# Optimization experiments

Measured on AMD Instinct MI355X. Metric: run time of the kernel, lower is better.

The kernel has to match this reference:

```python
import jax, jax.numpy as jnp
import numpy as np

EPS = 1e-8
H = 4      # n_heads
W = 64     # mem_word_length


def _split_controls(controls):
    # per-head partition: [W, W, W, 1, 1, 3, 1]
    B = controls.shape[0]
    sizes = [W, W, W, 1, 1, 3, 1]
    parts, pos = [], 0
    for s in sizes:
        n = H * s
        parts.append(controls[:, pos:pos + n].reshape(B, H, s))
        pos += n
    return parts  # keys, erase_vec, write_vec, betas, gates, shifts, gammas


def _address_memory(memory, keys, betas, gates, shifts, gammas, prev_weights):
    keys = jnp.tanh(keys)                      # [B,H,W]
    betas = jax.nn.softplus(betas)             # [B,H,1]
    gates = jax.nn.sigmoid(gates)              # [B,H,1]
    shifts = jax.nn.softmax(shifts, axis=-1)   # [B,H,3]
    gammas = 1.0 + jax.nn.softplus(gammas)     # [B,H,1]

    # cosine similarity: [B,H,N]
    dots = jnp.einsum('bhw,bnw->bhn', keys, memory)
    norm = jnp.linalg.norm(keys, axis=-1, keepdims=True) \
         * jnp.linalg.norm(memory, axis=-1)[:, None, :]
    scores = dots / (norm + EPS)

    w_content = jax.nn.softmax(scores * betas, axis=-1)            # [B,H,N]
    w_interp = gates * w_content + (1.0 - gates) * prev_weights    # [B,H,N]

    # circular 3-tap shift: out[n] = s0*w[n-1] + s1*w[n] + s2*w[n+1]
    w_shift = (shifts[..., 0:1] * jnp.roll(w_interp, 1, axis=-1)
             + shifts[..., 1:2] * w_interp
             + shifts[..., 2:3] * jnp.roll(w_interp, -1, axis=-1))

    w_sharp = w_shift ** gammas
    return w_sharp / (jnp.sum(w_sharp, axis=-1, keepdims=True) + EPS)


def reference(memory, controls, prev_weights):
    keys, erase_vec, write_vec, betas, gates, shifts, gammas = _split_controls(controls)
    write_dist = _address_memory(memory, keys, betas, gates, shifts, gammas, prev_weights)  # [B,H,N]
    write_data = jnp.tanh(write_vec)       # [B,H,W]
    erase_data = jax.nn.sigmoid(erase_vec) # [B,H,W]

    # erase: prod over heads of (1 - w[b,h,n]*e[b,h,w]) -> [B,N,W]
    erase_matrix = jnp.prod(1.0 - write_dist[:, :, :, None] * erase_data[:, :, None, :], axis=1)
    update_matrix = jnp.einsum('bhn,bhw->bnw', write_dist, write_data)
    return memory * erase_matrix + update_matrix


def setup_inputs() -> dict:
    key = jax.random.key(0)
    k1, k2, k3 = jax.random.split(key, 3)
    B, N = 64, 8192
    memory = jax.random.normal(k1, (B, N, W), dtype=jnp.float32)
    controls = jax.random.normal(k2, (B, H * (3 * W + 6)), dtype=jnp.float32)
    prev_weights = jax.random.uniform(k3, (B, H, N), dtype=jnp.float32)
    return {"memory": memory, "controls": controls, "prev_weights": prev_weights}
```

## Files before the change

### kernel.cpp

```cpp
#include <hip/hip_runtime.h>
#include <math.h>

#define EPS 1e-8f

typedef float nfloat4 __attribute__((ext_vector_type(4)));

__device__ __forceinline__ float softplus_f(float x) {
    return (x > 20.0f) ? x : log1pf(expf(x));
}
__device__ __forceinline__ float sigmoid_f(float x) {
    return 1.0f / (1.0f + expf(-x));
}


__global__ __launch_bounds__(256)
void score_kernel(const float* __restrict__ memory,
                  const float* __restrict__ controls,
                  float* __restrict__ scores, int N)
{
    int b = blockIdx.y;
    int nbase = blockIdx.x * 128;
    int t = threadIdx.x;
    int rq = t >> 4;
    int lane = t & 15;

    __shared__ float kk[256];
    __shared__ float betas_s[4], knorm_s[4];
    __shared__ float sc[4][128];

    const float* c = controls + (size_t)b * 792;

    {
        int h = t >> 6, w = t & 63;
        float kt = tanhf(c[h * 64 + w]);
        kk[h * 64 + w] = kt;
        float nsq = kt * kt;
        #pragma unroll
        for (int m = 1; m < 64; m <<= 1) nsq += __shfl_xor(nsq, m, 64);
        if (w == 0) knorm_s[h] = sqrtf(nsq);
        if (t < 4)  betas_s[t] = softplus_f(c[768 + t]);
    }
    __syncthreads();

    float4 k4[4];
    #pragma unroll
    for (int h = 0; h < 4; h++) k4[h] = ((const float4*)(kk + h * 64))[lane];
    float beta_l[4], knorm_l[4];
    #pragma unroll
    for (int h = 0; h < 4; h++) { beta_l[h] = betas_s[h]; knorm_l[h] = knorm_s[h]; }

    float4 m4[8];
    #pragma unroll
    for (int j = 0; j < 8; j++) {
        int n = nbase + rq + 16 * j;
        m4[j] = ((const float4*)(memory + ((size_t)b * N + n) * 64))[lane];
    }

    #pragma unroll
    for (int j = 0; j < 8; j++) {
        float nsq = m4[j].x * m4[j].x + m4[j].y * m4[j].y
                  + m4[j].z * m4[j].z + m4[j].w * m4[j].w;
        float d[4];
        #pragma unroll
        for (int h = 0; h < 4; h++) {
            d[h] = m4[j].x * k4[h].x + m4[j].y * k4[h].y
                 + m4[j].z * k4[h].z + m4[j].w * k4[h].w;
        }
        #pragma unroll
        for (int m = 1; m < 16; m <<= 1) {
            nsq += __shfl_xor(nsq, m, 64);
            #pragma unroll
            for (int h = 0; h < 4; h++) d[h] += __shfl_xor(d[h], m, 64);
        }
        if (lane == 0) {
            float mn = sqrtf(nsq);
            int row = rq + 16 * j;
            #pragma unroll
            for (int h = 0; h < 4; h++)
                sc[h][row] = beta_l[h] * d[h] / (mn * knorm_l[h] + EPS);
        }
    }
    __syncthreads();
    #pragma unroll
    for (int k = 0; k < 2; k++) {
        int idx = t + k * 256;
        int h = idx >> 7, i = idx & 127;
        scores[((size_t)b * 4 + h) * N + nbase + i] = sc[h][i];
    }
}

__device__ __forceinline__ float block_reduce_sum(float v, float* red) {
    #pragma unroll
    for (int m = 1; m < 64; m <<= 1) v += __shfl_xor(v, m, 64);
    int wid = threadIdx.x >> 6;
    __syncthreads();
    if ((threadIdx.x & 63) == 0) red[wid] = v;
    __syncthreads();
    float r = red[0];
    #pragma unroll
    for (int i = 1; i < 16; i++) r += red[i];
    return r;
}
__device__ __forceinline__ float block_reduce_max(float v, float* red) {
    #pragma unroll
    for (int m = 1; m < 64; m <<= 1) v = fmaxf(v, __shfl_xor(v, m, 64));
    int wid = threadIdx.x >> 6;
    __syncthreads();
    if ((threadIdx.x & 63) == 0) red[wid] = v;
    __syncthreads();
    float r = red[0];
    #pragma unroll
    for (int i = 1; i < 16; i++) r = fmaxf(r, red[i]);
    return r;
}

__global__ __launch_bounds__(1024)
void weights_kernel(float* __restrict__ scores,
                    const float* __restrict__ prev,
                    const float* __restrict__ controls, int N)
{
    int bh = blockIdx.x;
    int b = bh >> 2, h = bh & 3;
    int t = threadIdx.x;
    const float* c = controls + (size_t)b * 792;

    float gate  = sigmoid_f(c[772 + h]);
    float r0 = c[776 + h * 3 + 0];
    float r1 = c[776 + h * 3 + 1];
    float r2 = c[776 + h * 3 + 2];
    float rmx = fmaxf(r0, fmaxf(r1, r2));
    float e0 = expf(r0 - rmx), e1 = expf(r1 - rmx), e2 = expf(r2 - rmx);
    float sinv = 1.0f / (e0 + e1 + e2);
    float s0 = e0 * sinv, s1 = e1 * sinv, s2 = e2 * sinv;
    float gamma = 1.0f + softplus_f(c[788 + h]);

    __shared__ float wi_s[8192];
    __shared__ float red[16];

    float* srow = scores + (size_t)bh * N;
    const float* prow = prev + (size_t)bh * N;
    int half = N >> 1;
    int i0 = 4 * t, i1 = half + 4 * t;

    float4 sa = ((const float4*)srow)[t];
    float4 sb = ((const float4*)srow)[half / 4 + t];
    float4 pa = ((const float4*)prow)[t];
    float4 pb = ((const float4*)prow)[half / 4 + t];

    float mx = fmaxf(fmaxf(fmaxf(sa.x, sa.y), fmaxf(sa.z, sa.w)),
                     fmaxf(fmaxf(sb.x, sb.y), fmaxf(sb.z, sb.w)));
    mx = block_reduce_max(mx, red);

    float ea[4] = { __expf(sa.x - mx), __expf(sa.y - mx), __expf(sa.z - mx), __expf(sa.w - mx) };
    float eb[4] = { __expf(sb.x - mx), __expf(sb.y - mx), __expf(sb.z - mx), __expf(sb.w - mx) };
    float lsum = ea[0] + ea[1] + ea[2] + ea[3] + eb[0] + eb[1] + eb[2] + eb[3];
    float S = block_reduce_sum(lsum, red);
    float invS = 1.0f / S;

    float og = 1.0f - gate;
    float pv_a[4] = { pa.x, pa.y, pa.z, pa.w };
    float pv_b[4] = { pb.x, pb.y, pb.z, pb.w };
    #pragma unroll
    for (int k = 0; k < 4; k++) {
        wi_s[i0 + k] = gate * (ea[k] * invS) + og * pv_a[k];
        wi_s[i1 + k] = gate * (eb[k] * invS) + og * pv_b[k];
    }
    __syncthreads();

    float wsv[8]; float lsum2 = 0.0f;
    #pragma unroll
    for (int cc = 0; cc < 2; cc++) {
        int base = (cc == 0) ? i0 : i1;
        #pragma unroll
        for (int k = 0; k < 4; k++) {
            int i = base + k;
            int im1 = (i == 0) ? (N - 1) : (i - 1);
            int ip1 = (i == N - 1) ? 0 : (i + 1);
            float ws = s0 * wi_s[im1] + s1 * wi_s[i] + s2 * wi_s[ip1];
            float wp = __expf(gamma * __logf(ws));
            wsv[cc * 4 + k] = wp; lsum2 += wp;
        }
    }
    float T = block_reduce_sum(lsum2, red);
    float invT = 1.0f / (T + EPS);

    float4 oa = make_float4(wsv[0] * invT, wsv[1] * invT, wsv[2] * invT, wsv[3] * invT);
    float4 ob = make_float4(wsv[4] * invT, wsv[5] * invT, wsv[6] * invT, wsv[7] * invT);
    ((float4*)srow)[t] = oa;
    ((float4*)srow)[half / 4 + t] = ob;
}

__global__ __launch_bounds__(256)
void output_kernel(const float* __restrict__ memory,
                   const float* __restrict__ wdist,
                   const float* __restrict__ controls,
                   float* __restrict__ out, int N)
{
    int t = threadIdx.x;
    int blocksPerB = N >> 7;
    int b = blockIdx.x / blocksPerB;
    int nbase = (blockIdx.x % blocksPerB) << 7;

    __shared__ float es[256], wv[256], wd_s[512];
    const float* c = controls + (size_t)b * 792;
    es[t] = sigmoid_f(c[256 + t]);
    wv[t] = tanhf(c[512 + t]);
    #pragma unroll
    for (int k = 0; k < 2; k++) {
        int idx = t + k * 256;
        int h = idx >> 7, i = idx & 127;
        wd_s[idx] = wdist[((size_t)b * 4 + h) * N + nbase + i];
    }
    __syncthreads();

    int rq = t >> 4, lane = t & 15;

    float4 e4[4], w4[4];
    #pragma unroll
    for (int h = 0; h < 4; h++) {
        e4[h] = ((const float4*)(es + h * 64))[lane];
        w4[h] = ((const float4*)(wv + h * 64))[lane];
    }

    float4 m4[8];
    #pragma unroll
    for (int j = 0; j < 8; j++) {
        int n = nbase + rq + 16 * j;
        m4[j] = ((const float4*)(memory + ((size_t)b * N + n) * 64))[lane];
    }

    #pragma unroll
    for (int j = 0; j < 8; j++) {
        int row = rq + 16 * j;
        int n = nbase + row;
        float4 pe = make_float4(1.f, 1.f, 1.f, 1.f);
        float4 up = make_float4(0.f, 0.f, 0.f, 0.f);
        #pragma unroll
        for (int h = 0; h < 4; h++) {
            float f = wd_s[h * 128 + row];
            pe.x *= 1.0f - f * e4[h].x;  pe.y *= 1.0f - f * e4[h].y;
            pe.z *= 1.0f - f * e4[h].z;  pe.w *= 1.0f - f * e4[h].w;
            up.x += f * w4[h].x;  up.y += f * w4[h].y;
            up.z += f * w4[h].z;  up.w += f * w4[h].w;
        }
        nfloat4 o;
        o.x = m4[j].x * pe.x + up.x;
        o.y = m4[j].y * pe.y + up.y;
        o.z = m4[j].z * pe.z + up.z;
        o.w = m4[j].w * pe.w + up.w;
        nfloat4* op = ((nfloat4*)(out + ((size_t)b * N + n) * 64)) + lane;
        __builtin_nontemporal_store(o, op);
    }
}

extern "C" void kernel_launch(void* const* d_in, const int* in_sizes, int n_in,
                              void* d_out, int out_size, void* d_ws, size_t ws_size,
                              hipStream_t stream) {
    const float* memory   = (const float*)d_in[0];
    const float* controls = (const float*)d_in[1];
    const float* prev     = (const float*)d_in[2];
    float* out = (float*)d_out;

    int B = in_sizes[1] / 792;
    int N = in_sizes[0] / (B * 64);

    float* scores = (float*)d_ws;

    score_kernel<<<dim3(N / 128, B), 256, 0, stream>>>(memory, controls, scores, N);
    weights_kernel<<<B * 4, 1024, 0, stream>>>(scores, prev, controls, N);
    output_kernel<<<B * (N / 128), 256, 0, stream>>>(memory, scores, controls, out, N);
}
```

Baseline: 268.5 us.

## Drop softmax max pass and split weight stage across chunked blocks

Uses the fact that cosine similarity scaled by beta is bounded by beta, so exponentials are computed as exp(s-beta) directly in the score kernel, along with per-tile partial sums. This removes the global max reduction. The weights stage is split into many 2048-element chunks with halo loads and partial sharpening sums, and the final normalization moves into the output kernel. This increases parallelism for the sequential per-head stage, at the cost of extra partial-sum buffers and a small risk of underflow when beta is large.

Measured after the change: 263.8 us. No clear change (-1.7%).

```diff
diff --git a/kernel.cpp b/kernel.cpp
--- a/kernel.cpp
+++ b/kernel.cpp
@@ -16,13 +16,16 @@
 __global__ __launch_bounds__(256)
 void score_kernel(const float* __restrict__ memory,
                   const float* __restrict__ controls,
-                  float* __restrict__ scores, int N)
+                  float* __restrict__ evals,
+                  float* __restrict__ S_part, int N)
 {
     int b = blockIdx.y;
-    int nbase = blockIdx.x * 128;
+    int tile = blockIdx.x;
+    int nbase = tile * 128;
     int t = threadIdx.x;
     int rq = t >> 4;
     int lane = t & 15;
+    int ntiles = N >> 7;
 
     __shared__ float kk[256];
     __shared__ float betas_s[4], knorm_s[4];
@@ -76,53 +79,57 @@
             float mn = sqrtf(nsq);
             int row = rq + 16 * j;
             #pragma unroll
-            for (int h = 0; h < 4; h++)
-                sc[h][row] = beta_l[h] * d[h] / (mn * knorm_l[h] + EPS);
-        }
-    }
-    __syncthreads();
+            for (int h = 0; h < 4; h++) {
+                float s = beta_l[h] * d[h] / (mn * knorm_l[h] + EPS);
+                sc[h][row] = __expf(s - beta_l[h]);
+            }
+        }
+    }
+    __syncthreads();
+
     #pragma unroll
     for (int k = 0; k < 2; k++) {
         int idx = t + k * 256;
         int h = idx >> 7, i = idx & 127;
-        scores[((size_t)b * 4 + h) * N + nbase + i] = sc[h][i];
-    }
-}
-
-__device__ __forceinline__ float block_reduce_sum(float v, float* red) {
-    #pragma unroll
-    for (int m = 1; m < 64; m <<= 1) v += __shfl_xor(v, m, 64);
-    int wid = threadIdx.x >> 6;
-    __syncthreads();
-    if ((threadIdx.x & 63) == 0) red[wid] = v;
-    __syncthreads();
-    float r = red[0];
-    #pragma unroll
-    for (int i = 1; i < 16; i++) r += red[i];
-    return r;
-}
-__device__ __forceinline__ float block_reduce_max(float v, float* red) {
-    #pragma unroll
-    for (int m = 1; m < 64; m <<= 1) v = fmaxf(v, __shfl_xor(v, m, 64));
-    int wid = threadIdx.x >> 6;
-    __syncthreads();
-    if ((threadIdx.x & 63) == 0) red[wid] = v;
-    __syncthreads();
-    float r = red[0];
-    #pragma unroll
-    for (int i = 1; i < 16; i++) r = fmaxf(r, red[i]);
-    return r;
-}
-
-__global__ __launch_bounds__(1024)
-void weights_kernel(float* __restrict__ scores,
-                    const float* __restrict__ prev,
-                    const float* __restrict__ controls, int N)
+        evals[((size_t)b * 4 + h) * N + nbase + i] = sc[h][i];
+    }
+
+    {
+        int h = t >> 6, w = t & 63;
+        float v = sc[h][w] + sc[h][w + 64];
+        #pragma unroll
+        for (int m = 1; m < 64; m <<= 1) v += __shfl_xor(v, m, 64);
+        if (w == 0) S_part[((size_t)b * 4 + h) * ntiles + tile] = v;
+    }
+}
+
+__global__ __launch_bounds__(256)
+void shift_kernel(const float* __restrict__ evals,
+                  const float* __restrict__ prev,
+                  const float* __restrict__ controls,
+                  const float* __restrict__ S_part,
+                  float* __restrict__ wp,
+                  float* __restrict__ T_part, int N)
 {
-    int bh = blockIdx.x;
+    int CH = N >> 11;
+    int bh = blockIdx.x / CH;
+    int chunk = blockIdx.x - bh * CH;
     int b = bh >> 2, h = bh & 3;
     int t = threadIdx.x;
+    int ntiles = N >> 7;
     const float* c = controls + (size_t)b * 792;
+
+    __shared__ float wl[2050];
+    __shared__ float redm[4];
+    __shared__ float Ssh;
+
+    if (t < 64) {
+        float v = 0.0f;
+        for (int i = t; i < ntiles; i += 64) v += S_part[(size_t)bh * ntiles + i];
+        #pragma unroll
+        for (int m = 1; m < 64; m <<= 1) v += __shfl_xor(v, m, 64);
+        if (t == 0) Ssh = v;
+    }
 
     float gate  = sigmoid_f(c[772 + h]);
     float r0 = c[776 + h * 3 + 0];
@@ -134,65 +141,73 @@
     float s0 = e0 * sinv, s1 = e1 * sinv, s2 = e2 * sinv;
     float gamma = 1.0f + softplus_f(c[788 + h]);
 
-    __shared__ float wi_s[8192];
-    __shared__ float red[16];
-
-    float* srow = scores + (size_t)bh * N;
-    const float* prow = prev + (size_t)bh * N;
-    int half = N >> 1;
-    int i0 = 4 * t, i1 = half + 4 * t;
-
-    float4 sa = ((const float4*)srow)[t];
-    float4 sb = ((const float4*)srow)[half / 4 + t];
-    float4 pa = ((const float4*)prow)[t];
-    float4 pb = ((const float4*)prow)[half / 4 + t];
-
-    float mx = fmaxf(fmaxf(fmaxf(sa.x, sa.y), fmaxf(sa.z, sa.w)),
-                     fmaxf(fmaxf(sb.x, sb.y), fmaxf(sb.z, sb.w)));
-    mx = block_reduce_max(mx, red);
-
-    float ea[4] = { __expf(sa.x - mx), __expf(sa.y - mx), __expf(sa.z - mx), __expf(sa.w - mx) };
-    float eb[4] = { __expf(sb.x - mx), __expf(sb.y - mx), __expf(sb.z - mx), __expf(sb.w - mx) };
-    float lsum = ea[0] + ea[1] + ea[2] + ea[3] + eb[0] + eb[1] + eb[2] + eb[3];
-    float S = block_reduce_sum(lsum, red);
-    float invS = 1.0f / S;
-
+    const float* erow = evals + (size_t)bh * N;
+    const float* prow = prev  + (size_t)bh * N;
+    int base = chunk << 11;
+    int li = t << 3;
+
+    float4 ea = ((const float4*)(erow + base))[2 * t];
+    float4 eb = ((const float4*)(erow + base))[2 * t + 1];
+    float4 pa = ((const float4*)(prow + base))[2 * t];
+    float4 pb = ((const float4*)(prow + base))[2 * t + 1];
+
+    __syncthreads();
+    float invS = 1.0f / Ssh;
     float og = 1.0f - gate;
-    float pv_a[4] = { pa.x, pa.y, pa.z, pa.w };
-    float pv_b[4] = { pb.x, pb.y, pb.z, pb.w };
-    #pragma unroll
-    for (int k = 0; k < 4; k++) {
-        wi_s[i0 + k] = gate * (ea[k] * invS) + og * pv_a[k];
-        wi_s[i1 + k] = gate * (eb[k] * invS) + og * pv_b[k];
-    }
-    __syncthreads();
-
-    float wsv[8]; float lsum2 = 0.0f;
-    #pragma unroll
-    for (int cc = 0; cc < 2; cc++) {
-        int base = (cc == 0) ? i0 : i1;
-        #pragma unroll
-        for (int k = 0; k < 4; k++) {
-            int i = base + k;
-            int im1 = (i == 0) ? (N - 1) : (i - 1);
-            int ip1 = (i == N - 1) ? 0 : (i + 1);
-            float ws = s0 * wi_s[im1] + s1 * wi_s[i] + s2 * wi_s[ip1];
-            float wp = __expf(gamma * __logf(ws));
-            wsv[cc * 4 + k] = wp; lsum2 += wp;
-        }
-    }
-    float T = block_reduce_sum(lsum2, red);
-    float invT = 1.0f / (T + EPS);
-
-    float4 oa = make_float4(wsv[0] * invT, wsv[1] * invT, wsv[2] * invT, wsv[3] * invT);
-    float4 ob = make_float4(wsv[4] * invT, wsv[5] * invT, wsv[6] * invT, wsv[7] * invT);
-    ((float4*)srow)[t] = oa;
-    ((float4*)srow)[half / 4 + t] = ob;
+
+    float w[8];
+    w[0] = gate * ea.x * invS + og * pa.x;
+    w[1] = gate * ea.y * invS + og * pa.y;
+    w[2] = gate * ea.z * invS + og * pa.z;
+    w[3] = gate * ea.w * invS + og * pa.w;
+    w[4] = gate * eb.x * invS + og * pb.x;
+    w[5] = gate * eb.y * invS + og * pb.y;
+    w[6] = gate * eb.z * invS + og * pb.z;
+    w[7] = gate * eb.w * invS + og * pb.w;
+
+    #pragma unroll
+    for (int k = 0; k < 8; k++) wl[1 + li + k] = w[k];
+    if (t == 0) {
+        int g = base - 1; if (g < 0) g += N;
+        wl[0] = gate * erow[g] * invS + og * prow[g];
+    }
+    if (t == 255) {
+        int g = base + 2048; if (g >= N) g -= N;
+        wl[2049] = gate * erow[g] * invS + og * prow[g];
+    }
+    __syncthreads();
+
+    float nb[10];
+    nb[0] = wl[li];
+    #pragma unroll
+    for (int k = 0; k < 8; k++) nb[k + 1] = w[k];
+    nb[9] = wl[li + 9];
+
+    float o[8];
+    float acc = 0.0f;
+    #pragma unroll
+    for (int k = 0; k < 8; k++) {
+        float ws = s0 * nb[k] + s1 * nb[k + 1] + s2 * nb[k + 2];
+        float v = __expf(gamma * __logf(ws));
+        o[k] = v; acc += v;
+    }
+
+    #pragma unroll
+    for (int m = 1; m < 64; m <<= 1) acc += __shfl_xor(acc, m, 64);
+    if ((t & 63) == 0) redm[t >> 6] = acc;
+    __syncthreads();
+    if (t == 0) T_part[(size_t)bh * CH + chunk] = redm[0] + redm[1] + redm[2] + redm[3];
+
+    float4 oa = make_float4(o[0], o[1], o[2], o[3]);
+    float4 ob = make_float4(o[4], o[5], o[6], o[7]);
+    ((float4*)(wp + (size_t)bh * N + base))[2 * t] = oa;
+    ((float4*)(wp + (size_t)bh * N + base))[2 * t + 1] = ob;
 }
 
 __global__ __launch_bounds__(256)
 void output_kernel(const float* __restrict__ memory,
                    const float* __restrict__ wdist,
+                   const float* __restrict__ T_part,
                    const float* __restrict__ controls,
                    float* __restrict__ out, int N)
 {
@@ -200,16 +215,23 @@
     int blocksPerB = N >> 7;
     int b = blockIdx.x / blocksPerB;
     int nbase = (blockIdx.x % blocksPerB) << 7;
-
-    __shared__ float es[256], wv[256], wd_s[512];
+    int CH = N >> 11;
+
+    __shared__ float es[256], wv[256], wd_s[512], invT_s[4];
     const float* c = controls + (size_t)b * 792;
+    if (t < 4) {
+        float s = 0.0f;
+        for (int cc = 0; cc < CH; cc++) s += T_part[((size_t)b * 4 + t) * CH + cc];
+        invT_s[t] = 1.0f / (s + EPS);
+    }
     es[t] = sigmoid_f(c[256 + t]);
     wv[t] = tanhf(c[512 + t]);
+    __syncthreads();
     #pragma unroll
     for (int k = 0; k < 2; k++) {
         int idx = t + k * 256;
         int h = idx >> 7, i = idx & 127;
-        wd_s[idx] = wdist[((size_t)b * 4 + h) * N + nbase + i];
+        wd_s[idx] = wdist[((size_t)b * 4 + h) * N + nbase + i] * invT_s[h];
     }
     __syncthreads();
 
@@ -263,10 +285,15 @@
 
     int B = in_sizes[1] / 792;
     int N = in_sizes[0] / (B * 64);
-
-    float* scores = (float*)d_ws;
-
-    score_kernel<<<dim3(N / 128, B), 256, 0, stream>>>(memory, controls, scores, N);
-    weights_kernel<<<B * 4, 1024, 0, stream>>>(scores, prev, controls, N);
-    output_kernel<<<B * (N / 128), 256, 0, stream>>>(memory, scores, controls, out, N);
-}
+    int ntiles = N >> 7;
+    int CH = N >> 11;
+
+    float* evals  = (float*)d_ws;
+    float* wp     = evals + (size_t)B * 4 * N;
+    float* S_part = wp + (size_t)B * 4 * N;
+    float* T_part = S_part + (size_t)B * 4 * ntiles;
+
+    score_kernel<<<dim3(ntiles, B), 256, 0, stream>>>(memory, controls, evals, S_part, N);
+    shift_kernel<<<B * 4 * CH, 256, 0, stream>>>(evals, prev, controls, S_part, wp, T_part, N);
+    output_kernel<<<B * ntiles, 256, 0, stream>>>(memory, wp, T_part, controls, out, N);
+}
```

## Fuse three kernels into one persistent kernel with grid barriers

Applied to the files above, without the earlier changes.

Replaces the score, weights and output kernels with one kernel that processes 8 tiles per block. Per-tile exp values stay in shared memory across the phases, and the softmax and sharpen normalisations use per-tile partial sums with two software grid barriers. The 3-tap shift crosses tile edges through stored boundary values and a halo. This removes the global score round trip and the low-parallelism weights kernel. The kernel depends on all 512 blocks being co-resident (256 threads, launch bounds 2 per CU), and the softmax uses beta as a fixed max offset instead of the true max. Memory is still read twice.

New measurement: 463.4 us. +72.6%, slower.

```diff
diff --git a/kernel.cpp b/kernel.cpp
--- a/kernel.cpp
+++ b/kernel.cpp
@@ -2,6 +2,7 @@
 #include <math.h>
 
 #define EPS 1e-8f
+#define UMAX 8
 
 typedef float nfloat4 __attribute__((ext_vector_type(4)));
 
@@ -12,244 +13,267 @@
     return 1.0f / (1.0f + expf(-x));
 }
 
-
-__global__ __launch_bounds__(256)
-void score_kernel(const float* __restrict__ memory,
-                  const float* __restrict__ controls,
-                  float* __restrict__ scores, int N)
-{
-    int b = blockIdx.y;
-    int nbase = blockIdx.x * 128;
-    int t = threadIdx.x;
-    int rq = t >> 4;
-    int lane = t & 15;
-
-    __shared__ float kk[256];
-    __shared__ float betas_s[4], knorm_s[4];
-    __shared__ float sc[4][128];
-
-    const float* c = controls + (size_t)b * 792;
-
-    {
-        int h = t >> 6, w = t & 63;
-        float kt = tanhf(c[h * 64 + w]);
-        kk[h * 64 + w] = kt;
-        float nsq = kt * kt;
-        #pragma unroll
-        for (int m = 1; m < 64; m <<= 1) nsq += __shfl_xor(nsq, m, 64);
-        if (w == 0) knorm_s[h] = sqrtf(nsq);
-        if (t < 4)  betas_s[t] = softplus_f(c[768 + t]);
+__device__ __forceinline__ void grid_barrier(unsigned* cnt, unsigned* gen, unsigned nb) {
+    __syncthreads();
+    if (threadIdx.x == 0) {
+        __threadfence();
+        unsigned g = __hip_atomic_load(gen, __ATOMIC_RELAXED, __HIP_MEMORY_SCOPE_AGENT);
+        unsigned arrived = __hip_atomic_fetch_add(cnt, 1u, __ATOMIC_ACQ_REL, __HIP_MEMORY_SCOPE_AGENT);
+        if (arrived == nb - 1u) {
+            __hip_atomic_store(cnt, 0u, __ATOMIC_RELAXED, __HIP_MEMORY_SCOPE_AGENT);
+            __hip_atomic_fetch_add(gen, 1u, __ATOMIC_RELEASE, __HIP_MEMORY_SCOPE_AGENT);
+        } else {
+            int tries = 0;
+            while (__hip_atomic_load(gen, __ATOMIC_ACQUIRE, __HIP_MEMORY_SCOPE_AGENT) == g) {
+                __builtin_amdgcn_s_sleep(2);
+                if (++tries > (1 << 24)) break;
+            }
+        }
+        __threadfence();
     }
     __syncthreads();
-
-    float4 k4[4];
-    #pragma unroll
-    for (int h = 0; h < 4; h++) k4[h] = ((const float4*)(kk + h * 64))[lane];
-    float beta_l[4], knorm_l[4];
-    #pragma unroll
-    for (int h = 0; h < 4; h++) { beta_l[h] = betas_s[h]; knorm_l[h] = knorm_s[h]; }
-
-    float4 m4[8];
-    #pragma unroll
-    for (int j = 0; j < 8; j++) {
-        int n = nbase + rq + 16 * j;
-        m4[j] = ((const float4*)(memory + ((size_t)b * N + n) * 64))[lane];
+}
+
+__global__ void init_barrier(unsigned* bar) {
+    __hip_atomic_store(bar + 0, 0u, __ATOMIC_RELAXED, __HIP_MEMORY_SCOPE_AGENT);
+    __hip_atomic_store(bar + 1, 0u, __ATOMIC_RELAXED, __HIP_MEMORY_SCOPE_AGENT);
+}
+
+__global__ __launch_bounds__(256, 2)
+void fused_kernel(const float* __restrict__ memory,
+                  const float* __restrict__ controls,
+                  const float* __restrict__ prev,
+                  float* __restrict__ out,
+                  unsigned* __restrict__ bar,
+                  float* __restrict__ S_part,
+                  float* __restrict__ ebnd,
+                  float* __restrict__ T_part,
+                  int N, int B, unsigned nblocks)
+{
+    const int t = threadIdx.x;
+    const int ntiles = N >> 7;
+    const int totalUnits = B * ntiles;
+
+    __shared__ __align__(16) float e_wp[UMAX][4][128];
+    __shared__ __align__(16) float kk[256];
+    __shared__ __align__(16) float scratch[520];
+    __shared__ float knorm_s[4], betas_s[4];
+    __shared__ float scal_gate[4], scal_og[4], scal_s0[4], scal_s1[4], scal_s2[4], scal_gm[4];
+    __shared__ float halo_e[8], halo_p[8];
+    __shared__ float Ssh[4], invT_s[4];
+
+    for (int u = 0; u < UMAX; u++) {
+        int uid = blockIdx.x * UMAX + u;
+        if (uid >= totalUnits) break;
+        int b = uid / ntiles, tile = uid - b * ntiles;
+        int nbase = tile << 7;
+        const float* c = controls + (size_t)b * 792;
+
+        __syncthreads();
+        {
+            int h = t >> 6, w = t & 63;
+            float kt = tanhf(c[h * 64 + w]);
+            kk[h * 64 + w] = kt;
+            float nsq = kt * kt;
+            #pragma unroll
+            for (int m = 1; m < 64; m <<= 1) nsq += __shfl_xor(nsq, m, 64);
+            if (w == 0) knorm_s[h] = sqrtf(nsq);
+            if (t < 4)  betas_s[t] = softplus_f(c[768 + t]);
+        }
+        __syncthreads();
+
+        int rq = t >> 4, lane = t & 15;
+        float4 k4[4];
+        #pragma unroll
+        for (int h = 0; h < 4; h++) k4[h] = ((const float4*)(kk + h * 64))[lane];
+        float beta_l[4], kn_l[4];
+        #pragma unroll
+        for (int h = 0; h < 4; h++) { beta_l[h] = betas_s[h]; kn_l[h] = knorm_s[h]; }
+
+        float4 m4[8];
+        #pragma unroll
+        for (int j = 0; j < 8; j++) {
+            int n = nbase + rq + 16 * j;
+            m4[j] = ((const float4*)(memory + ((size_t)b * N + n) * 64))[lane];
+        }
+        #pragma unroll
+        for (int j = 0; j < 8; j++) {
+            float nsq = m4[j].x * m4[j].x + m4[j].y * m4[j].y
+                      + m4[j].z * m4[j].z + m4[j].w * m4[j].w;
+            float d[4];
+            #pragma unroll
+            for (int h = 0; h < 4; h++)
+                d[h] = m4[j].x * k4[h].x + m4[j].y * k4[h].y
+                     + m4[j].z * k4[h].z + m4[j].w * k4[h].w;
+            #pragma unroll
+            for (int m = 1; m < 16; m <<= 1) {
+                nsq += __shfl_xor(nsq, m, 64);
+                #pragma unroll
+                for (int h = 0; h < 4; h++) d[h] += __shfl_xor(d[h], m, 64);
+            }
+            if (lane == 0) {
+                float mn = sqrtf(nsq);
+                int row = rq + 16 * j;
+                #pragma unroll
+                for (int h = 0; h < 4; h++) {
+                    float s = beta_l[h] * d[h] / (mn * kn_l[h] + EPS);
+                    e_wp[u][h][row] = __expf(s - beta_l[h]);
+                }
+            }
+        }
+        __syncthreads();
+        {
+            int h = t >> 6, w = t & 63;
+            float v = e_wp[u][h][w] + e_wp[u][h][w + 64];
+            #pragma unroll
+            for (int m = 1; m < 64; m <<= 1) v += __shfl_xor(v, m, 64);
+            if (w == 0) S_part[((size_t)b * 4 + h) * ntiles + tile] = v;
+        }
+        if (t < 8) {
+            int hh = t >> 1, side = t & 1;
+            ebnd[(size_t)uid * 8 + hh * 2 + side] = e_wp[u][hh][side ? 127 : 0];
+        }
     }
 
-    #pragma unroll
-    for (int j = 0; j < 8; j++) {
-        float nsq = m4[j].x * m4[j].x + m4[j].y * m4[j].y
-                  + m4[j].z * m4[j].z + m4[j].w * m4[j].w;
-        float d[4];
+    grid_barrier(bar, bar + 1, nblocks);
+
+    for (int u = 0; u < UMAX; u++) {
+        int uid = blockIdx.x * UMAX + u;
+        if (uid >= totalUnits) break;
+        int b = uid / ntiles, tile = uid - b * ntiles;
+        int nbase = tile << 7;
+        const float* c = controls + (size_t)b * 792;
+        float* wiS = scratch;
+
+        __syncthreads();
+        {
+            int h = t >> 6, w = t & 63;
+            float v = 0.0f;
+            for (int i = w; i < ntiles; i += 64)
+                v += S_part[((size_t)b * 4 + h) * ntiles + i];
+            #pragma unroll
+            for (int m = 1; m < 64; m <<= 1) v += __shfl_xor(v, m, 64);
+            if (w == 0) Ssh[h] = v;
+        }
+        if (t < 4) {
+            int h = t;
+            float g = sigmoid_f(c[772 + h]);
+            scal_gate[h] = g; scal_og[h] = 1.0f - g;
+            float r0 = c[776 + h * 3], r1 = c[776 + h * 3 + 1], r2 = c[776 + h * 3 + 2];
+            float rmx = fmaxf(r0, fmaxf(r1, r2));
+            float e0 = expf(r0 - rmx), e1 = expf(r1 - rmx), e2 = expf(r2 - rmx);
+            float si = 1.0f / (e0 + e1 + e2);
+            scal_s0[h] = e0 * si; scal_s1[h] = e1 * si; scal_s2[h] = e2 * si;
+            scal_gm[h] = 1.0f + softplus_f(c[788 + h]);
+        }
+        if (t < 8) {
+            int h = t >> 1, side = t & 1;
+            int g = side ? nbase + 128 : nbase - 1;
+            if (g < 0) g += N; if (g >= N) g -= N;
+            int gt = g >> 7, gr = g & 127;
+            halo_e[t] = ebnd[(size_t)(b * ntiles + gt) * 8 + h * 2 + (gr == 127 ? 1 : 0)];
+            halo_p[t] = prev[((size_t)b * 4 + h) * N + g];
+        }
+        __syncthreads();
+
+        int h0 = t >> 7, row = t & 127, h1 = h0 + 2;
+        {
+            float i0 = 1.0f / Ssh[h0], i1 = 1.0f / Ssh[h1];
+            float p0 = prev[((size_t)b * 4 + h0) * N + nbase + row];
+            float p1 = prev[((size_t)b * 4 + h1) * N + nbase + row];
+            wiS[h0 * 130 + row + 1] = scal_gate[h0] * e_wp[u][h0][row] * i0 + scal_og[h0] * p0;
+            wiS[h1 * 130 + row + 1] = scal_gate[h1] * e_wp[u][h1][row] * i1 + scal_og[h1] * p1;
+        }
+        if (t < 8) {
+            int h = t >> 1, side = t & 1;
+            wiS[h * 130 + (side ? 129 : 0)] =
+                scal_gate[h] * halo_e[t] * (1.0f / Ssh[h]) + scal_og[h] * halo_p[t];
+        }
+        __syncthreads();
+        {
+            float ws0 = scal_s0[h0] * wiS[h0 * 130 + row]
+                      + scal_s1[h0] * wiS[h0 * 130 + row + 1]
+                      + scal_s2[h0] * wiS[h0 * 130 + row + 2];
+            float ws1 = scal_s0[h1] * wiS[h1 * 130 + row]
+                      + scal_s1[h1] * wiS[h1 * 130 + row + 1]
+                      + scal_s2[h1] * wiS[h1 * 130 + row + 2];
+            e_wp[u][h0][row] = __expf(scal_gm[h0] * __logf(ws0));
+            e_wp[u][h1][row] = __expf(scal_gm[h1] * __logf(ws1));
+        }
+        __syncthreads();
+        {
+            int h = t >> 6, w = t & 63;
+            float v = e_wp[u][h][w] + e_wp[u][h][w + 64];
+            #pragma unroll
+            for (int m = 1; m < 64; m <<= 1) v += __shfl_xor(v, m, 64);
+            if (w == 0) T_part[((size_t)b * 4 + h) * ntiles + tile] = v;
+        }
+    }
+
+    grid_barrier(bar, bar + 1, nblocks);
+
+    for (int u = 0; u < UMAX; u++) {
+        int uid = blockIdx.x * UMAX + u;
+        if (uid >= totalUnits) break;
+        int b = uid / ntiles, tile = uid - b * ntiles;
+        int nbase = tile << 7;
+        const float* c = controls + (size_t)b * 792;
+        float* es_s = scratch;
+        float* wv_s = scratch + 260;
+
+        __syncthreads();
+        {
+            int h = t >> 6, w = t & 63;
+            float v = 0.0f;
+            for (int i = w; i < ntiles; i += 64)
+                v += T_part[((size_t)b * 4 + h) * ntiles + i];
+            #pragma unroll
+            for (int m = 1; m < 64; m <<= 1) v += __shfl_xor(v, m, 64);
+            if (w == 0) invT_s[h] = 1.0f / (v + EPS);
+        }
+        es_s[t] = sigmoid_f(c[256 + t]);
+        wv_s[t] = tanhf(c[512 + t]);
+        __syncthreads();
+
+        int rq = t >> 4, lane = t & 15;
+        float4 e4[4], w4[4];
         #pragma unroll
         for (int h = 0; h < 4; h++) {
-            d[h] = m4[j].x * k4[h].x + m4[j].y * k4[h].y
-                 + m4[j].z * k4[h].z + m4[j].w * k4[h].w;
-        }
-        #pragma unroll
-        for (int m = 1; m < 16; m <<= 1) {
-            nsq += __shfl_xor(nsq, m, 64);
-            #pragma unroll
-            for (int h = 0; h < 4; h++) d[h] += __shfl_xor(d[h], m, 64);
-        }
-        if (lane == 0) {
-            float mn = sqrtf(nsq);
+            e4[h] = ((const float4*)(es_s + h * 64))[lane];
+            w4[h] = ((const float4*)(wv_s + h * 64))[lane];
+        }
+        float invT_l[4];
+        #pragma unroll
+        for (int h = 0; h < 4; h++) invT_l[h] = invT_s[h];
+
+        float4 m4[8];
+        #pragma unroll
+        for (int j = 0; j < 8; j++) {
+            int n = nbase + rq + 16 * j;
+            m4[j] = ((const float4*)(memory + ((size_t)b * N + n) * 64))[lane];
+        }
+        #pragma unroll
+        for (int j = 0; j < 8; j++) {
             int row = rq + 16 * j;
-            #pragma unroll
-            for (int h = 0; h < 4; h++)
-                sc[h][row] = beta_l[h] * d[h] / (mn * knorm_l[h] + EPS);
-        }
-    }
-    __syncthreads();
-    #pragma unroll
-    for (int k = 0; k < 2; k++) {
-        int idx = t + k * 256;
-        int h = idx >> 7, i = idx & 127;
-        scores[((size_t)b * 4 + h) * N + nbase + i] = sc[h][i];
-    }
-}
-
-__device__ __forceinline__ float block_reduce_sum(float v, float* red) {
-    #pragma unroll
-    for (int m = 1; m < 64; m <<= 1) v += __shfl_xor(v, m, 64);
-    int wid = threadIdx.x >> 6;
-    __syncthreads();
-    if ((threadIdx.x & 63) == 0) red[wid] = v;
-    __syncthreads();
-    float r = red[0];
-    #pragma unroll
-    for (int i = 1; i < 16; i++) r += red[i];
-    return r;
-}
-__device__ __forceinline__ float block_reduce_max(float v, float* red) {
-    #pragma unroll
-    for (int m = 1; m < 64; m <<= 1) v = fmaxf(v, __shfl_xor(v, m, 64));
-    int wid = threadIdx.x >> 6;
-    __syncthreads();
-    if ((threadIdx.x & 63) == 0) red[wid] = v;
-    __syncthreads();
-    float r = red[0];
-    #pragma unroll
-    for (int i = 1; i < 16; i++) r = fmaxf(r, red[i]);
-    return r;
-}
-
-__global__ __launch_bounds__(1024)
-void weights_kernel(float* __restrict__ scores,
-                    const float* __restrict__ prev,
-                    const float* __restrict__ controls, int N)
-{
-    int bh = blockIdx.x;
-    int b = bh >> 2, h = bh & 3;
-    int t = threadIdx.x;
-    const float* c = controls + (size_t)b * 792;
-
-    float gate  = sigmoid_f(c[772 + h]);
-    float r0 = c[776 + h * 3 + 0];
-    float r1 = c[776 + h * 3 + 1];
-    float r2 = c[776 + h * 3 + 2];
-    float rmx = fmaxf(r0, fmaxf(r1, r2));
-    float e0 = expf(r0 - rmx), e1 = expf(r1 - rmx), e2 = expf(r2 - rmx);
-    float sinv = 1.0f / (e0 + e1 + e2);
-    float s0 = e0 * sinv, s1 = e1 * sinv, s2 = e2 * sinv;
-    float gamma = 1.0f + softplus_f(c[788 + h]);
-
-    __shared__ float wi_s[8192];
-    __shared__ float red[16];
-
-    float* srow = scores + (size_t)bh * N;
-    const float* prow = prev + (size_t)bh * N;
-    int half = N >> 1;
-    int i0 = 4 * t, i1 = half + 4 * t;
-
-    float4 sa = ((const float4*)srow)[t];
-    float4 sb = ((const float4*)srow)[half / 4 + t];
-    float4 pa = ((const float4*)prow)[t];
-    float4 pb = ((const float4*)prow)[half / 4 + t];
-
-    float mx = fmaxf(fmaxf(fmaxf(sa.x, sa.y), fmaxf(sa.z, sa.w)),
-                     fmaxf(fmaxf(sb.x, sb.y), fmaxf(sb.z, sb.w)));
-    mx = block_reduce_max(mx, red);
-
-    float ea[4] = { __expf(sa.x - mx), __expf(sa.y - mx), __expf(sa.z - mx), __expf(sa.w - mx) };
-    float eb[4] = { __expf(sb.x - mx), __expf(sb.y - mx), __expf(sb.z - mx), __expf(sb.w - mx) };
-    float lsum = ea[0] + ea[1] + ea[2] + ea[3] + eb[0] + eb[1] + eb[2] + eb[3];
-    float S = block_reduce_sum(lsum, red);
-    float invS = 1.0f / S;
-
-    float og = 1.0f - gate;
-    float pv_a[4] = { pa.x, pa.y, pa.z, pa.w };
-    float pv_b[4] = { pb.x, pb.y, pb.z, pb.w };
-    #pragma unroll
-    for (int k = 0; k < 4; k++) {
-        wi_s[i0 + k] = gate * (ea[k] * invS) + og * pv_a[k];
-        wi_s[i1 + k] = gate * (eb[k] * invS) + og * pv_b[k];
-    }
-    __syncthreads();
-
-    float wsv[8]; float lsum2 = 0.0f;
-    #pragma unroll
-    for (int cc = 0; cc < 2; cc++) {
-        int base = (cc == 0) ? i0 : i1;
-        #pragma unroll
-        for (int k = 0; k < 4; k++) {
-            int i = base + k;
-            int im1 = (i == 0) ? (N - 1) : (i - 1);
-            int ip1 = (i == N - 1) ? 0 : (i + 1);
-            float ws = s0 * wi_s[im1] + s1 * wi_s[i] + s2 * wi_s[ip1];
-            float wp = __expf(gamma * __logf(ws));
-            wsv[cc * 4 + k] = wp; lsum2 += wp;
-        }
-    }
-    float T = block_reduce_sum(lsum2, red);
-    float invT = 1.0f / (T + EPS);
-
-    float4 oa = make_float4(wsv[0] * invT, wsv[1] * invT, wsv[2] * invT, wsv[3] * invT);
-    float4 ob = make_float4(wsv[4] * invT, wsv[5] * invT, wsv[6] * invT, wsv[7] * invT);
-    ((float4*)srow)[t] = oa;
-    ((float4*)srow)[half / 4 + t] = ob;
-}
-
-__global__ __launch_bounds__(256)
-void output_kernel(const float* __restrict__ memory,
-                   const float* __restrict__ wdist,
-                   const float* __restrict__ controls,
-                   float* __restrict__ out, int N)
-{
-    int t = threadIdx.x;
-    int blocksPerB = N >> 7;
-    int b = blockIdx.x / blocksPerB;
-    int nbase = (blockIdx.x % blocksPerB) << 7;
-
-    __shared__ float es[256], wv[256], wd_s[512];
-    const float* c = controls + (size_t)b * 792;
-    es[t] = sigmoid_f(c[256 + t]);
-    wv[t] = tanhf(c[512 + t]);
-    #pragma unroll
-    for (int k = 0; k < 2; k++) {
-        int idx = t + k * 256;
-        int h = idx >> 7, i = idx & 127;
-        wd_s[idx] = wdist[((size_t)b * 4 + h) * N + nbase + i];
-    }
-    __syncthreads();
-
-    int rq = t >> 4, lane = t & 15;
-
-    float4 e4[4], w4[4];
-    #pragma unroll
-    for (int h = 0; h < 4; h++) {
-        e4[h] = ((const float4*)(es + h * 64))[lane];
-        w4[h] = ((const float4*)(wv + h * 64))[lane];
-    }
-
-    float4 m4[8];
-    #pragma unroll
-    for (int j = 0; j < 8; j++) {
-        int n = nbase + rq + 16 * j;
-        m4[j] = ((const float4*)(memory + ((size_t)b * N + n) * 64))[lane];
-    }
-
-    #pragma unroll
-    for (int j = 0; j < 8; j++) {
-        int row = rq + 16 * j;
-        int n = nbase + row;
-        float4 pe = make_float4(1.f, 1.f, 1.f, 1.f);
-        float4 up = make_float4(0.f, 0.f, 0.f, 0.f);
-        #pragma unroll
-        for (int h = 0; h < 4; h++) {
-            float f = wd_s[h * 128 + row];
-            pe.x *= 1.0f - f * e4[h].x;  pe.y *= 1.0f - f * e4[h].y;
-            pe.z *= 1.0f - f * e4[h].z;  pe.w *= 1.0f - f * e4[h].w;
-            up.x += f * w4[h].x;  up.y += f * w4[h].y;
-            up.z += f * w4[h].z;  up.w += f * w4[h].w;
-        }
-        nfloat4 o;
-        o.x = m4[j].x * pe.x + up.x;
-        o.y = m4[j].y * pe.y + up.y;
-        o.z = m4[j].z * pe.z + up.z;
-        o.w = m4[j].w * pe.w + up.w;
-        nfloat4* op = ((nfloat4*)(out + ((size_t)b * N + n) * 64)) + lane;
-        __builtin_nontemporal_store(o, op);
+            int n = nbase + row;
+            float4 pe = make_float4(1.f, 1.f, 1.f, 1.f);
+            float4 up = make_float4(0.f, 0.f, 0.f, 0.f);
+            #pragma unroll
+            for (int h = 0; h < 4; h++) {
+                float f = e_wp[u][h][row] * invT_l[h];
+                pe.x *= 1.0f - f * e4[h].x;  pe.y *= 1.0f - f * e4[h].y;
+                pe.z *= 1.0f - f * e4[h].z;  pe.w *= 1.0f - f * e4[h].w;
+                up.x += f * w4[h].x;  up.y += f * w4[h].y;
+                up.z += f * w4[h].z;  up.w += f * w4[h].w;
+            }
+            nfloat4 o;
+            o.x = m4[j].x * pe.x + up.x;
+            o.y = m4[j].y * pe.y + up.y;
+            o.z = m4[j].z * pe.z + up.z;
+            o.w = m4[j].w * pe.w + up.w;
+            nfloat4* op = ((nfloat4*)(out + ((size_t)b * N + n) * 64)) + lane;
+            __builtin_nontemporal_store(o, op);
+        }
     }
 }
 
@@ -263,10 +287,16 @@
 
     int B = in_sizes[1] / 792;
     int N = in_sizes[0] / (B * 64);
-
-    float* scores = (float*)d_ws;
-
-    score_kernel<<<dim3(N / 128, B), 256, 0, stream>>>(memory, controls, scores, N);
-    weights_kernel<<<B * 4, 1024, 0, stream>>>(scores, prev, controls, N);
-    output_kernel<<<B * (N / 128), 256, 0, stream>>>(memory, scores, controls, out, N);
-}
+    int ntiles = N >> 7;
+    int totalUnits = B * ntiles;
+    unsigned nblocks = (unsigned)((totalUnits + UMAX - 1) / UMAX);
+
+    unsigned* bar = (unsigned*)d_ws;
+    float* S_part = (float*)d_ws + 16;
+    float* T_part = S_part + (size_t)B * 4 * ntiles;
+    float* ebnd   = T_part + (size_t)B * 4 * ntiles;
+
+    init_barrier<<<1, 1, 0, stream>>>(bar);
+    fused_kernel<<<dim3(nblocks), dim3(256), 0, stream>>>(
+        memory, controls, prev, out, bar, S_part, ebnd, T_part, N, B, nblocks);
+}
```
